# Kernel optimization log

Measured on AMD Instinct MI355X. Metric: run time of the kernel, lower is better.

Reference implementation:

```python
import jax, jax.numpy as jnp
import numpy as np

B, T, D, L = 64, 512, 1024, 32


def setup_inputs() -> dict:
    key = jax.random.key(0)
    ks = jax.random.split(key, 6)
    x = jax.random.normal(ks[0], (B, T, D), jnp.float32)
    W = jax.random.normal(ks[1], (D, L), jnp.float32) * 0.02  # TruncatedNormal(stddev=0.02) analogue
    b = jnp.zeros((L,), jnp.float32)
    transitions = jax.random.normal(ks[2], (L, L), jnp.float32) * 0.1
    label = jax.random.randint(ks[3], (B, T), 0, L).astype(jnp.int32)
    seqlen = jax.random.randint(ks[4], (B,), 1, T + 1).astype(jnp.int32)
    mask = jnp.arange(T)[None, :] < seqlen[:, None]
    return {"x": x, "W": W, "b": b, "transitions": transitions,
            "label": label, "seqlen": seqlen, "mask": mask}


def crf_sequence_score(emissions, label, seqlen, transitions):
    # emissions: [B,T,L]
    Bc, Tc, Lc = emissions.shape
    m = (jnp.arange(Tc)[None, :] < seqlen[:, None]).astype(emissions.dtype)  # [B,T]
    unary = jnp.take_along_axis(emissions, label[..., None].astype(jnp.int32), axis=-1)[..., 0]
    unary = jnp.sum(unary * m, axis=1)
    trans = transitions[label[:, :-1], label[:, 1:]]  # [B,T-1]
    mt = (jnp.arange(1, Tc)[None, :] < seqlen[:, None]).astype(emissions.dtype)
    binary = jnp.sum(trans * mt, axis=1)
    return unary + binary


def crf_log_norm(emissions, seqlen, transitions):
    Bc, Tc, Lc = emissions.shape
    alpha0 = emissions[:, 0]  # [B,L]
    valid = (jnp.arange(1, Tc)[None, :] < seqlen[:, None]).T  # [T-1,B]
    emits = jnp.moveaxis(emissions[:, 1:], 1, 0)  # [T-1,B,L]

    def step(alpha, inp):
        emit_t, v = inp
        new = jax.nn.logsumexp(alpha[:, :, None] + transitions[None], axis=1) + emit_t
        return jnp.where(v[:, None], new, alpha), None

    alpha, _ = jax.lax.scan(step, alpha0, (emits, valid))
    return jax.nn.logsumexp(alpha, axis=-1)  # [B]


def crf_decode(emissions, transitions, seqlen):
    Bc, Tc, Lc = emissions.shape
    alpha0 = emissions[:, 0]
    idx = jnp.arange(Lc, dtype=jnp.int32)
    valid = (jnp.arange(1, Tc)[None, :] < seqlen[:, None]).T  # [T-1,B]
    emits = jnp.moveaxis(emissions[:, 1:], 1, 0)

    def fwd(alpha, inp):
        emit_t, v = inp
        scores = alpha[:, :, None] + transitions[None]  # [B,L,L]
        best = jnp.max(scores, axis=1) + emit_t
        bp = jnp.argmax(scores, axis=1).astype(jnp.int32)  # [B,L]
        alpha_new = jnp.where(v[:, None], best, alpha)
        bp = jnp.where(v[:, None], bp, idx[None, :])  # identity bp on padded steps
        return alpha_new, bp

    alpha, bps = jax.lax.scan(fwd, alpha0, (emits, valid))  # bps: [T-1,B,L]
    last = jnp.argmax(alpha, axis=-1).astype(jnp.int32)  # [B]

    def bwd(tag, bp):
        prev = jnp.take_along_axis(bp, tag[:, None], axis=1)[:, 0]
        return prev, tag

    first, tags = jax.lax.scan(bwd, last, bps, reverse=True)  # tags[i] = tag at t=i+1
    seq = jnp.concatenate([first[None], tags], axis=0)  # [T,B]
    return jnp.moveaxis(seq, 0, 1)  # [B,T]


def reference(x, W, b, transitions, label, seqlen, mask):
    emissions = jnp.einsum('btd,dl->btl', x, W) + b  # Dense projection
    ll = crf_sequence_score(emissions, label, seqlen, transitions) - crf_log_norm(emissions, seqlen, transitions)
    loss = jnp.mean(-ll)
    vit = crf_decode(emissions, transitions, seqlen)
    tp = jnp.sum(((label > 0) & (vit == label)).astype(jnp.float32))
    tn = jnp.sum(((label > 0) & (vit != label)).astype(jnp.float32))
    fp = jnp.sum((mask & (label == 0) & (vit > 0)).astype(jnp.float32))
    return loss, vit, tp, tn, fp
```

## Files before the change

### kernel.cpp

```cpp
#include <hip/hip_runtime.h>
#include <stdint.h>
#include <math.h>

#define Bn 64
#define Tn 512
#define Dn 1024
#define Ln 32
#define LOG2E 1.4426950408889634f
#define LN2f  0.6931471805599453f

#define EMIS_OFF 0
#define LOGNORM_OFF (Bn * Tn * Ln)
#define SCORE_OFF (LOGNORM_OFF + Bn)
#define CNT_OFF (SCORE_OFF + Bn)

#define MAX3(a,b,c) fmaxf(fmaxf((a),(b)),(c))

template<int K>
__device__ __forceinline__ float rorf(float v) {
    return __int_as_float(__builtin_amdgcn_update_dpp(
        0, __float_as_int(v), 0x120 | K, 0xF, 0xF, true));
}

__device__ __forceinline__ float opaque_copy(float v) {
    float r;
    asm("v_mov_b32 %0, %1" : "=v"(r) : "v"(v));
    return r;
}

__device__ __forceinline__ void swap32p(float p, float& x, float& y) {
    x = p;
    y = opaque_copy(p);
    asm("v_permlane32_swap_b32 %0, %1" : "+v"(x), "+v"(y));
}
__device__ __forceinline__ void swap16p(float p, float& x, float& y) {
    x = p;
    y = opaque_copy(p);
    asm("v_permlane16_swap_b32 %0, %1" : "+v"(x), "+v"(y));
}

#define BM 128
#define KB 32
#define XSS 132

__global__ __launch_bounds__(256) void gemm_emis(
    const float* __restrict__ x, const float* __restrict__ Wm,
    const float* __restrict__ bias, const int* __restrict__ seqlen,
    float* __restrict__ emis)
{
    int b  = blockIdx.x >> 2;
    int t0 = (blockIdx.x & 3) * BM;
    if (t0 >= seqlen[b]) return;

    __shared__ __align__(16) float xs[KB * XSS];
    __shared__ __align__(16) float wsh[KB * Ln];

    int tid = threadIdx.x;
    int cg = tid & 7;
    int rg = tid >> 3;

    const float* xrow = x + (size_t)(b * Tn + t0) * Dn;

    float acc[4][4];
    #pragma unroll
    for (int z = 0; z < 4; z++)
        #pragma unroll
        for (int c = 0; c < 4; c++) acc[z][c] = 0.f;

    float4 xr[4]; float4 wr;
    #pragma unroll
    for (int u = 0; u < 4; u++) {
        int f = tid + 256 * u;
        xr[u] = *(const float4*)(xrow + (size_t)(f >> 3) * Dn + (f & 7) * 4);
    }
    wr = *(const float4*)(Wm + tid * 4);

    for (int k0 = 0; k0 < Dn; k0 += KB) {
        __syncthreads();
        #pragma unroll
        for (int u = 0; u < 4; u++) {
            int f = tid + 256 * u;
            int lrow = f >> 3, kk = f & 7;
            xs[(4 * kk + 0) * XSS + lrow] = xr[u].x;
            xs[(4 * kk + 1) * XSS + lrow] = xr[u].y;
            xs[(4 * kk + 2) * XSS + lrow] = xr[u].z;
            xs[(4 * kk + 3) * XSS + lrow] = xr[u].w;
        }
        *(float4*)(wsh + tid * 4) = wr;
        __syncthreads();

        int kn = k0 + KB;
        if (kn < Dn) {
            #pragma unroll
            for (int u = 0; u < 4; u++) {
                int f = tid + 256 * u;
                xr[u] = *(const float4*)(xrow + (size_t)(f >> 3) * Dn + kn + (f & 7) * 4);
            }
            wr = *(const float4*)(Wm + (size_t)kn * Ln + tid * 4);
        }

        #pragma unroll 8
        for (int k = 0; k < KB; k++) {
            float4 a = *(const float4*)(xs + k * XSS + 4 * rg);
            float4 w = *(const float4*)(wsh + k * Ln + 4 * cg);
            float av[4] = {a.x, a.y, a.z, a.w};
            float wv[4] = {w.x, w.y, w.z, w.w};
            #pragma unroll
            for (int z = 0; z < 4; z++)
                #pragma unroll
                for (int c = 0; c < 4; c++)
                    acc[z][c] = fmaf(av[z], wv[c], acc[z][c]);
        }
    }

    float4 bv = *(const float4*)(bias + 4 * cg);
    float bb[4] = {bv.x, bv.y, bv.z, bv.w};
    #pragma unroll
    for (int z = 0; z < 4; z++) {
        float4 o;
        o.x = acc[z][0] + bb[0];
        o.y = acc[z][1] + bb[1];
        o.z = acc[z][2] + bb[2];
        o.w = acc[z][3] + bb[3];
        *(float4*)(emis + (size_t)(b * Tn + t0 + 4 * rg + z) * Ln + 4 * cg) = o;
    }
}

#define CH 64

#define VIT_BODY(T, TRARR, SWAPFN, OE)                                       \
  {                                                                          \
    int tnx2 = ((T) + 2 < slen) ? ((T) + 2) : (slen - 1);                    \
    float e2n = es[tnx2 * Ln + (OE)];                                        \
    float vv0  = av            + TRARR[0];                                   \
    float vv1  = rorf<1>(av)   + TRARR[1];                                   \
    float vv2  = rorf<2>(av)   + TRARR[2];                                   \
    float vv3  = rorf<3>(av)   + TRARR[3];                                   \
    float vv4  = rorf<4>(av)   + TRARR[4];                                   \
    float vv5  = rorf<5>(av)   + TRARR[5];                                   \
    float vv6  = rorf<6>(av)   + TRARR[6];                                   \
    float vv7  = rorf<7>(av)   + TRARR[7];                                   \
    float vv8  = rorf<8>(av)   + TRARR[8];                                   \
    float vv9  = rorf<9>(av)   + TRARR[9];                                   \
    float vv10 = rorf<10>(av)  + TRARR[10];                                  \
    float vv11 = rorf<11>(av)  + TRARR[11];                                  \
    float vv12 = rorf<12>(av)  + TRARR[12];                                  \
    float vv13 = rorf<13>(av)  + TRARR[13];                                  \
    float vv14 = rorf<14>(av)  + TRARR[14];                                  \
    float vv15 = rorf<15>(av)  + TRARR[15];                                  \
    float g0 = MAX3(vv0,  vv1,  vv2);                                        \
    float g1 = MAX3(vv3,  vv4,  vv5);                                        \
    float g2 = MAX3(vv6,  vv7,  vv8);                                        \
    float g3 = MAX3(vv9,  vv10, vv11);                                       \
    float g4 = MAX3(vv12, vv13, vv14);                                       \
    float h0 = MAX3(g0, g1, g2);                                             \
    float h1 = MAX3(g3, g4, vv15);                                           \
    float p = fmaxf(h0, h1);                                                 \
    float xx, yy; SWAPFN(p, xx, yy);                                         \
    float cmb = fmaxf(xx, yy) + emit;                                        \
    al[(T) * Ln + (OE)] = cmb;                                               \
    av = cmb;                                                                \
    emit = emitn; emitn = e2n;                                               \
  }

#define LSE_BODY(T, EARR, SWAPFN, OE, DORENORM)                              \
  {                                                                          \
    int tnx2 = ((T) + 2 < slen) ? ((T) + 2) : (slen - 1);                    \
    float rawn = es[tnx2 * Ln + (OE)];                                       \
    float een = exp2f(rawnext * LOG2E);                                      \
    float s0 = a           * EARR[0];                                        \
    float s1 = rorf<1>(a)  * EARR[1];                                        \
    float s2 = rorf<2>(a)  * EARR[2];                                        \
    float s3 = rorf<3>(a)  * EARR[3];                                        \
    s0 = fmaf(rorf<4>(a),  EARR[4],  s0);                                    \
    s1 = fmaf(rorf<5>(a),  EARR[5],  s1);                                    \
    s2 = fmaf(rorf<6>(a),  EARR[6],  s2);                                    \
    s3 = fmaf(rorf<7>(a),  EARR[7],  s3);                                    \
    s0 = fmaf(rorf<8>(a),  EARR[8],  s0);                                    \
    s1 = fmaf(rorf<9>(a),  EARR[9],  s1);                                    \
    s2 = fmaf(rorf<10>(a), EARR[10], s2);                                    \
    s3 = fmaf(rorf<11>(a), EARR[11], s3);                                    \
    s0 = fmaf(rorf<12>(a), EARR[12], s0);                                    \
    s1 = fmaf(rorf<13>(a), EARR[13], s1);                                    \
    s2 = fmaf(rorf<14>(a), EARR[14], s2);                                    \
    s3 = fmaf(rorf<15>(a), EARR[15], s3);                                    \
    float pp = (s0 + s1) + (s2 + s3);                                        \
    float xx, yy; SWAPFN(pp, xx, yy);                                        \
    float s = (xx + yy) * eemit;                                             \
    if ((DORENORM) && (((T) & 3) == 0)) {                                    \
        unsigned sb = (unsigned)__builtin_amdgcn_readfirstlane(__float_as_int(s)); \
        int e = (int)((sb >> 23) & 0xFFu) - 127;                             \
        Eacc += e;                                                           \
        a = ldexpf(s, -e);                                                   \
    } else {                                                                 \
        a = s;                                                               \
    }                                                                        \
    eemit = een; rawnext = rawn;                                             \
  }

__global__ __launch_bounds__(512) void crf_forward(
    const float* __restrict__ emis, const float* __restrict__ trans,
    const int* __restrict__ label, const int* __restrict__ seqlen,
    float* __restrict__ out, float* __restrict__ wsf)
{
    __shared__ __align__(16) float es[Tn * Ln];
    __shared__ __align__(16) float al[Tn * Ln];
    __shared__ __align__(16) float trs[Ln * Ln];
    __shared__ uint8_t bp[Tn * Ln];
    __shared__ uint8_t Fm[16 * 32];
    __shared__ int btag[16];
    __shared__ int s_last;
    __shared__ float credA[8], credB[8], credC[8];

    int tid = threadIdx.x;
    int b = blockIdx.x;
    int slen = seqlen[b];
    int wv = tid >> 6;
    int lane = tid & 63;
    int j = lane & 31;

    const float* eb = emis + (size_t)b * Tn * Ln;

    {
        int n4 = slen * (Ln / 4);
        for (int i4 = tid; i4 < n4; i4 += 512)
            ((float4*)es)[i4] = ((const float4*)eb)[i4];
    }
    if (tid < 256) ((float4*)trs)[tid] = ((const float4*)trans)[tid];
    {
        uint32_t* bp32 = (uint32_t*)bp;
        for (int w = tid; w < Tn * Ln / 4; w += 512)
            bp32[w] = 0x03020100u + 0x04040404u * (uint32_t)(w & 7);
    }

    int rq[16];
    {
        float qf = (float)(lane & 15);
        rq[0]  = lane & 15;
        rq[1]  = (int)rorf<1>(qf);   rq[2]  = (int)rorf<2>(qf);
        rq[3]  = (int)rorf<3>(qf);   rq[4]  = (int)rorf<4>(qf);
        rq[5]  = (int)rorf<5>(qf);   rq[6]  = (int)rorf<6>(qf);
        rq[7]  = (int)rorf<7>(qf);   rq[8]  = (int)rorf<8>(qf);
        rq[9]  = (int)rorf<9>(qf);   rq[10] = (int)rorf<10>(qf);
        rq[11] = (int)rorf<11>(qf);  rq[12] = (int)rorf<12>(qf);
        rq[13] = (int)rorf<13>(qf);  rq[14] = (int)rorf<14>(qf);
        rq[15] = (int)rorf<15>(qf);
    }
    int q4  = lane & 15;
    int sb4 = (lane & 16) ? 16 : 0;
    int sb5 = (lane & 32) ? 16 : 0;
    int o4  = q4 + sb4;
    int o5  = q4 + sb5;

    __syncthreads();

    float av = 0.f, emit = 0.f, emitn = 0.f;
    float a = 0.f, eemit = 0.f, rawnext = 0.f;
    int   Eacc = 0;
    float trA[16], trB[16];
    float e2A[16], e2B[16];
    float trH[32];

    int i1 = (1 < slen) ? 1 : (slen - 1);
    int i2 = (2 < slen) ? 2 : (slen - 1);

    if (wv == 0) {
        #pragma unroll
        for (int k = 0; k < 16; k++) {
            trA[k] = trs[(rq[k] + sb5) * Ln + o4];
            trB[k] = trs[(rq[k] + sb4) * Ln + o5];
        }
        av = es[o5];
        al[o5] = av;
        emit  = es[i1 * Ln + o4];
        emitn = es[i2 * Ln + o5];
    } else if (wv == 1) {
        #pragma unroll
        for (int k = 0; k < 16; k++) {
            e2A[k] = exp2f(trs[(rq[k] + sb5) * Ln + o4] * LOG2E);
            e2B[k] = exp2f(trs[(rq[k] + sb4) * Ln + o5] * LOG2E);
        }
        a = exp2f(es[o5] * LOG2E);
        eemit   = exp2f(es[i1 * Ln + o4] * LOG2E);
        rawnext = es[i2 * Ln + o5];
    } else {
        #pragma unroll
        for (int i = 0; i < 32; i++) trH[i] = trs[i * Ln + j];
    }

    for (int c = 0; c < Tn / CH; c++) {
        int tb = (c == 0) ? 1 : c * CH;
        int te = (c + 1) * CH; if (te > slen) te = slen;

        if (wv == 0) {
            int t = tb;
            if ((t & 1) && t < te) { VIT_BODY(t, trA, swap32p, o4); t++; }
            for (; t + 1 < te; t += 2) {
                VIT_BODY(t,     trB, swap16p, o5);
                VIT_BODY(t + 1, trA, swap32p, o4);
            }
            if (t < te) { VIT_BODY(t, trB, swap16p, o5); }
        } else if (wv == 1) {
            int t = tb;
            if ((t & 1) && t < te) { LSE_BODY(t, e2A, swap32p, o4, 0); t++; }
            for (; t + 1 < te; t += 2) {
                LSE_BODY(t,     e2B, swap16p, o5, 1);
                LSE_BODY(t + 1, e2A, swap32p, o4, 0);
            }
            if (t < te) { LSE_BODY(t, e2B, swap16p, o5, 1); }
        } else if (c == 0) {
            if (wv == 2) {
                const int* lb = label + (size_t)b * Tn;
                float acc = 0.f;
                for (int t = lane; t < Tn; t += 64) {
                    if (t < slen) {
                        int lc = lb[t];
                        acc += es[t * Ln + lc];
                        if (t >= 1) acc += trs[lb[t - 1] * Ln + lc];
                    }
                }
                #pragma unroll
                for (int off = 32; off >= 1; off >>= 1) acc += __shfl_xor(acc, off);
                if (lane == 0) wsf[SCORE_OFF + b] = acc;
            }
        } else {
            int stripe = (wv - 2) * 2 + (lane >> 5);
            int pb = ((c - 1) == 0) ? 1 : (c - 1) * CH;
            int pe = c * CH; if (pe > slen) pe = slen;
            for (int t = pb + stripe; t < pe; t += 12) {
                const float* ar = al + (t - 1) * Ln;
                float vv[32];
                #pragma unroll
                for (int i = 0; i < 32; i += 4) {
                    float4 a4 = *(const float4*)(ar + i);
                    vv[i]     = a4.x + trH[i];
                    vv[i + 1] = a4.y + trH[i + 1];
                    vv[i + 2] = a4.z + trH[i + 2];
                    vv[i + 3] = a4.w + trH[i + 3];
                }
                float mv[16]; int mi[16];
                #pragma unroll
                for (int i = 0; i < 16; i++) {
                    bool g = vv[2*i+1] > vv[2*i];
                    mv[i] = g ? vv[2*i+1] : vv[2*i];
                    mi[i] = g ? (2*i+1) : (2*i);
                }
                #pragma unroll
                for (int i = 0; i < 8; i++) {
                    bool g = mv[2*i+1] > mv[2*i];
                    mv[i] = g ? mv[2*i+1] : mv[2*i];
                    mi[i] = g ? mi[2*i+1] : mi[2*i];
                }
                #pragma unroll
                for (int i = 0; i < 4; i++) {
                    bool g = mv[2*i+1] > mv[2*i];
                    mv[i] = g ? mv[2*i+1] : mv[2*i];
                    mi[i] = g ? mi[2*i+1] : mi[2*i];
                }
                #pragma unroll
                for (int i = 0; i < 2; i++) {
                    bool g = mv[2*i+1] > mv[2*i];
                    mv[i] = g ? mv[2*i+1] : mv[2*i];
                    mi[i] = g ? mi[2*i+1] : mi[2*i];
                }
                bp[t * Ln + j] = (uint8_t)mi[0];
            }
        }
        __syncthreads();
    }

    if (wv == 0) {
        int oT = ((slen - 1) & 1) ? o4 : o5;
        float mm = av; int ai = oT;
        #pragma unroll
        for (int off = 32; off >= 1; off >>= 1) {
            float om = __shfl_xor(mm, off);
            int   oi = __shfl_xor(ai, off);
            if (om > mm || (om == mm && oi < ai)) { mm = om; ai = oi; }
        }
        if (lane == 0) s_last = ai;
    } else if (wv == 1) {
        float ss = a;
        #pragma unroll
        for (int off = 32; off >= 1; off >>= 1) ss += __shfl_xor(ss, off);
        if (lane == 0)
            wsf[LOGNORM_OFF + b] = (log2f(ss) - 1.0f + (float)Eacc) * LN2f;
    } else {
        int stripe = (wv - 2) * 2 + (lane >> 5);
        int cc = Tn / CH - 1;
        int pb = cc * CH;
        int pe = Tn; if (pe > slen) pe = slen;
        for (int t = pb + stripe; t < pe; t += 12) {
            const float* ar = al + (t - 1) * Ln;
            float vv[32];
            #pragma unroll
            for (int i = 0; i < 32; i += 4) {
                float4 a4 = *(const float4*)(ar + i);
                vv[i]     = a4.x + trH[i];
                vv[i + 1] = a4.y + trH[i + 1];
                vv[i + 2] = a4.z + trH[i + 2];
                vv[i + 3] = a4.w + trH[i + 3];
            }
            float mv[16]; int mi[16];
            #pragma unroll
            for (int i = 0; i < 16; i++) {
                bool g = vv[2*i+1] > vv[2*i];
                mv[i] = g ? vv[2*i+1] : vv[2*i];
                mi[i] = g ? (2*i+1) : (2*i);
            }
            #pragma unroll
            for (int i = 0; i < 8; i++) {
                bool g = mv[2*i+1] > mv[2*i];
                mv[i] = g ? mv[2*i+1] : mv[2*i];
                mi[i] = g ? mi[2*i+1] : mi[2*i];
            }
            #pragma unroll
            for (int i = 0; i < 4; i++) {
                bool g = mv[2*i+1] > mv[2*i];
                mv[i] = g ? mv[2*i+1] : mv[2*i];
                mi[i] = g ? mi[2*i+1] : mi[2*i];
            }
            #pragma unroll
            for (int i = 0; i < 2; i++) {
                bool g = mv[2*i+1] > mv[2*i];
                mv[i] = g ? mv[2*i+1] : mv[2*i];
                mi[i] = g ? mi[2*i+1] : mi[2*i];
            }
            bp[t * Ln + j] = (uint8_t)mi[0];
        }
    }
    __syncthreads();

    int sseg = tid >> 5, ent = tid & 31;
    {
        int y = ent;
        for (int p = 32 * sseg + 31; p >= 32 * sseg; p--) y = bp[p * Ln + y];
        Fm[sseg * 32 + ent] = (uint8_t)y;
    }
    __syncthreads();
    if (tid == 0) {
        int y = s_last;
        btag[15] = y;
        for (int ss = 15; ss >= 1; ss--) { y = Fm[ss * 32 + y]; btag[ss - 1] = y; }
    }
    __syncthreads();
    int q = tid;
    int y = btag[sseg];
    for (int p = 32 * sseg + 31; p >= q + 1; p--) y = bp[p * Ln + y];
    out[1 + (size_t)b * Tn + q] = (float)y;

    int lbl = label[(size_t)b * Tn + q];
    float tpf = (lbl > 0 && y == lbl) ? 1.f : 0.f;
    float tnf = (lbl > 0 && y != lbl) ? 1.f : 0.f;
    float fpf = (q < slen && lbl == 0 && y > 0) ? 1.f : 0.f;
    #pragma unroll
    for (int off = 32; off >= 1; off >>= 1) {
        tpf += __shfl_xor(tpf, off);
        tnf += __shfl_xor(tnf, off);
        fpf += __shfl_xor(fpf, off);
    }
    if (lane == 0) { credA[wv] = tpf; credB[wv] = tnf; credC[wv] = fpf; }
    __syncthreads();
    if (tid == 0) {
        float aa = 0.f, bb2 = 0.f, cc2 = 0.f;
        #pragma unroll
        for (int w = 0; w < 8; w++) { aa += credA[w]; bb2 += credB[w]; cc2 += credC[w]; }
        wsf[CNT_OFF + b] = aa;
        wsf[CNT_OFF + Bn + b] = bb2;
        wsf[CNT_OFF + 2 * Bn + b] = cc2;
    }
}

__global__ __launch_bounds__(64) void crf_final(const float* __restrict__ wsf,
                                                float* __restrict__ out)
{
    int lane = threadIdx.x;
    float nll = wsf[LOGNORM_OFF + lane] - wsf[SCORE_OFF + lane];
    float tp = wsf[CNT_OFF + lane];
    float tn = wsf[CNT_OFF + Bn + lane];
    float fp = wsf[CNT_OFF + 2 * Bn + lane];
    #pragma unroll
    for (int off = 32; off >= 1; off >>= 1) {
        nll += __shfl_xor(nll, off);
        tp  += __shfl_xor(tp, off);
        tn  += __shfl_xor(tn, off);
        fp  += __shfl_xor(fp, off);
    }
    if (lane == 0) {
        out[0] = nll * (1.f / 64.f);
        out[1 + Bn * Tn + 0] = tp;
        out[1 + Bn * Tn + 1] = tn;
        out[1 + Bn * Tn + 2] = fp;
    }
}

extern "C" void kernel_launch(void* const* d_in, const int* in_sizes, int n_in,
                              void* d_out, int out_size, void* d_ws, size_t ws_size,
                              hipStream_t stream) {
    const float* x     = (const float*)d_in[0];
    const float* W     = (const float*)d_in[1];
    const float* bias  = (const float*)d_in[2];
    const float* trans = (const float*)d_in[3];
    const int* label   = (const int*)d_in[4];
    const int* seqlen  = (const int*)d_in[5];
    float* out = (float*)d_out;
    float* wsf = (float*)d_ws;

    gemm_emis<<<dim3(Bn * (Tn / BM)), dim3(256), 0, stream>>>(x, W, bias, seqlen, wsf + EMIS_OFF);
    crf_forward<<<dim3(Bn), dim3(512), 0, stream>>>(wsf + EMIS_OFF, trans, label, seqlen, out, wsf);
    crf_final<<<dim3(1), dim3(64), 0, stream>>>(wsf, out);
}
```

Measured before the change: 271.7 us.

## Halve GEMM row tile and restrict backpointer work to four helper waves

The emission GEMM now uses 64-row tiles instead of 128. That doubles the grid to 512 blocks for better CU coverage and finer skipping of padded timesteps, at the cost of less register reuse per thread. In the CRF forward kernel, backpointer recomputation moves from six helper waves to four (waves 2,3,6,7) with stride 8, and waves 4 and 5 sit idle. This may reduce contention with the latency-critical recurrence waves, but it gives each helper lane more timesteps to process.

```diff
diff --git a/kernel.cpp b/kernel.cpp
--- a/kernel.cpp
+++ b/kernel.cpp
@@ -39,20 +39,20 @@
     asm("v_permlane16_swap_b32 %0, %1" : "+v"(x), "+v"(y));
 }
 
-#define BM 128
+#define BM2 64
 #define KB 32
-#define XSS 132
+#define XS2 68
 
 __global__ __launch_bounds__(256) void gemm_emis(
     const float* __restrict__ x, const float* __restrict__ Wm,
     const float* __restrict__ bias, const int* __restrict__ seqlen,
     float* __restrict__ emis)
 {
-    int b  = blockIdx.x >> 2;
-    int t0 = (blockIdx.x & 3) * BM;
+    int b  = blockIdx.x >> 3;
+    int t0 = (blockIdx.x & 7) * BM2;
     if (t0 >= seqlen[b]) return;
 
-    __shared__ __align__(16) float xs[KB * XSS];
+    __shared__ __align__(16) float xs[KB * XS2];
     __shared__ __align__(16) float wsh[KB * Ln];
 
     int tid = threadIdx.x;
@@ -61,15 +61,15 @@
 
     const float* xrow = x + (size_t)(b * Tn + t0) * Dn;
 
-    float acc[4][4];
+    float acc[2][4];
     #pragma unroll
-    for (int z = 0; z < 4; z++)
+    for (int z = 0; z < 2; z++)
         #pragma unroll
         for (int c = 0; c < 4; c++) acc[z][c] = 0.f;
 
-    float4 xr[4]; float4 wr;
+    float4 xr[2]; float4 wr;
     #pragma unroll
-    for (int u = 0; u < 4; u++) {
+    for (int u = 0; u < 2; u++) {
         int f = tid + 256 * u;
         xr[u] = *(const float4*)(xrow + (size_t)(f >> 3) * Dn + (f & 7) * 4);
     }
@@ -78,13 +78,13 @@
     for (int k0 = 0; k0 < Dn; k0 += KB) {
         __syncthreads();
         #pragma unroll
-        for (int u = 0; u < 4; u++) {
+        for (int u = 0; u < 2; u++) {
             int f = tid + 256 * u;
             int lrow = f >> 3, kk = f & 7;
-            xs[(4 * kk + 0) * XSS + lrow] = xr[u].x;
-            xs[(4 * kk + 1) * XSS + lrow] = xr[u].y;
-            xs[(4 * kk + 2) * XSS + lrow] = xr[u].z;
-            xs[(4 * kk + 3) * XSS + lrow] = xr[u].w;
+            xs[(4 * kk + 0) * XS2 + lrow] = xr[u].x;
+            xs[(4 * kk + 1) * XS2 + lrow] = xr[u].y;
+            xs[(4 * kk + 2) * XS2 + lrow] = xr[u].z;
+            xs[(4 * kk + 3) * XS2 + lrow] = xr[u].w;
         }
         *(float4*)(wsh + tid * 4) = wr;
         __syncthreads();
@@ -92,7 +92,7 @@
         int kn = k0 + KB;
         if (kn < Dn) {
             #pragma unroll
-            for (int u = 0; u < 4; u++) {
+            for (int u = 0; u < 2; u++) {
                 int f = tid + 256 * u;
                 xr[u] = *(const float4*)(xrow + (size_t)(f >> 3) * Dn + kn + (f & 7) * 4);
             }
@@ -101,12 +101,12 @@
 
         #pragma unroll 8
         for (int k = 0; k < KB; k++) {
-            float4 a = *(const float4*)(xs + k * XSS + 4 * rg);
+            float2 a2 = *(const float2*)(xs + k * XS2 + 2 * rg);
             float4 w = *(const float4*)(wsh + k * Ln + 4 * cg);
-            float av[4] = {a.x, a.y, a.z, a.w};
+            float av[2] = {a2.x, a2.y};
             float wv[4] = {w.x, w.y, w.z, w.w};
             #pragma unroll
-            for (int z = 0; z < 4; z++)
+            for (int z = 0; z < 2; z++)
                 #pragma unroll
                 for (int c = 0; c < 4; c++)
                     acc[z][c] = fmaf(av[z], wv[c], acc[z][c]);
@@ -116,13 +116,13 @@
     float4 bv = *(const float4*)(bias + 4 * cg);
     float bb[4] = {bv.x, bv.y, bv.z, bv.w};
     #pragma unroll
-    for (int z = 0; z < 4; z++) {
+    for (int z = 0; z < 2; z++) {
         float4 o;
         o.x = acc[z][0] + bb[0];
         o.y = acc[z][1] + bb[1];
         o.z = acc[z][2] + bb[2];
         o.w = acc[z][3] + bb[3];
-        *(float4*)(emis + (size_t)(b * Tn + t0 + 4 * rg + z) * Ln + 4 * cg) = o;
+        *(float4*)(emis + (size_t)(b * Tn + t0 + 2 * rg + z) * Ln + 4 * cg) = o;
     }
 }
 
@@ -198,6 +198,46 @@
     eemit = een; rawnext = rawn;                                             \
   }
 
+#define BP_LOOP(PB, PE, STRIDE)                                              \
+    for (int t = (PB); t < (PE); t += (STRIDE)) {                            \
+        const float* ar = al + (t - 1) * Ln;                                 \
+        float vv[32];                                                        \
+        _Pragma("unroll")                                                    \
+        for (int i = 0; i < 32; i += 4) {                                    \
+            float4 a4 = *(const float4*)(ar + i);                            \
+            vv[i]     = a4.x + trH[i];                                       \
+            vv[i + 1] = a4.y + trH[i + 1];                                   \
+            vv[i + 2] = a4.z + trH[i + 2];                                   \
+            vv[i + 3] = a4.w + trH[i + 3];                                   \
+        }                                                                    \
+        float mv[16]; int mi[16];                                            \
+        _Pragma("unroll")                                                    \
+        for (int i = 0; i < 16; i++) {                                       \
+            bool g = vv[2*i+1] > vv[2*i];                                    \
+            mv[i] = g ? vv[2*i+1] : vv[2*i];                                 \
+            mi[i] = g ? (2*i+1) : (2*i);                                     \
+        }                                                                    \
+        _Pragma("unroll")                                                    \
+        for (int i = 0; i < 8; i++) {                                        \
+            bool g = mv[2*i+1] > mv[2*i];                                    \
+            mv[i] = g ? mv[2*i+1] : mv[2*i];                                 \
+            mi[i] = g ? mi[2*i+1] : mi[2*i];                                 \
+        }                                                                    \
+        _Pragma("unroll")                                                    \
+        for (int i = 0; i < 4; i++) {                                        \
+            bool g = mv[2*i+1] > mv[2*i];                                    \
+            mv[i] = g ? mv[2*i+1] : mv[2*i];                                 \
+            mi[i] = g ? mi[2*i+1] : mi[2*i];                                 \
+        }                                                                    \
+        _Pragma("unroll")                                                    \
+        for (int i = 0; i < 2; i++) {                                        \
+            bool g = mv[2*i+1] > mv[2*i];                                    \
+            mv[i] = g ? mv[2*i+1] : mv[2*i];                                 \
+            mi[i] = g ? mi[2*i+1] : mi[2*i];                                 \
+        }                                                                    \
+        bp[t * Ln + j] = (uint8_t)mi[0];                                     \
+    }
+
 __global__ __launch_bounds__(512) void crf_forward(
     const float* __restrict__ emis, const float* __restrict__ trans,
     const int* __restrict__ label, const int* __restrict__ seqlen,
@@ -264,6 +304,10 @@
     int i1 = (1 < slen) ? 1 : (slen - 1);
     int i2 = (2 < slen) ? 2 : (slen - 1);
 
+    bool isHelper = (wv == 2) || (wv == 3) || (wv == 6) || (wv == 7);
+    int hw = (wv >= 6) ? (wv - 4) : (wv - 2);
+    int stripe = hw * 2 + (lane >> 5);
+
     if (wv == 0) {
         #pragma unroll
         for (int k = 0; k < 16; k++) {
@@ -283,7 +327,7 @@
         a = exp2f(es[o5] * LOG2E);
         eemit   = exp2f(es[i1 * Ln + o4] * LOG2E);
         rawnext = es[i2 * Ln + o5];
-    } else {
+    } else if (isHelper) {
         #pragma unroll
         for (int i = 0; i < 32; i++) trH[i] = trs[i * Ln + j];
     }
@@ -308,6 +352,7 @@
                 LSE_BODY(t + 1, e2A, swap32p, o4, 0);
             }
             if (t < te) { LSE_BODY(t, e2B, swap16p, o5, 1); }
+        } else if (!isHelper) {
         } else if (c == 0) {
             if (wv == 2) {
                 const int* lb = label + (size_t)b * Tn;
@@ -324,47 +369,9 @@
                 if (lane == 0) wsf[SCORE_OFF + b] = acc;
             }
         } else {
-            int stripe = (wv - 2) * 2 + (lane >> 5);
             int pb = ((c - 1) == 0) ? 1 : (c - 1) * CH;
             int pe = c * CH; if (pe > slen) pe = slen;
-            for (int t = pb + stripe; t < pe; t += 12) {
-                const float* ar = al + (t - 1) * Ln;
-                float vv[32];
-                #pragma unroll
-                for (int i = 0; i < 32; i += 4) {
-                    float4 a4 = *(const float4*)(ar + i);
-                    vv[i]     = a4.x + trH[i];
-                    vv[i + 1] = a4.y + trH[i + 1];
-                    vv[i + 2] = a4.z + trH[i + 2];
-                    vv[i + 3] = a4.w + trH[i + 3];
-                }
-                float mv[16]; int mi[16];
-                #pragma unroll
-                for (int i = 0; i < 16; i++) {
-                    bool g = vv[2*i+1] > vv[2*i];
-                    mv[i] = g ? vv[2*i+1] : vv[2*i];
-                    mi[i] = g ? (2*i+1) : (2*i);
-                }
-                #pragma unroll
-                for (int i = 0; i < 8; i++) {
-                    bool g = mv[2*i+1] > mv[2*i];
-                    mv[i] = g ? mv[2*i+1] : mv[2*i];
-                    mi[i] = g ? mi[2*i+1] : mi[2*i];
-                }
-                #pragma unroll
-                for (int i = 0; i < 4; i++) {
-                    bool g = mv[2*i+1] > mv[2*i];
-                    mv[i] = g ? mv[2*i+1] : mv[2*i];
-                    mi[i] = g ? mi[2*i+1] : mi[2*i];
-                }
-                #pragma unroll
-                for (int i = 0; i < 2; i++) {
-                    bool g = mv[2*i+1] > mv[2*i];
-                    mv[i] = g ? mv[2*i+1] : mv[2*i];
-                    mi[i] = g ? mi[2*i+1] : mi[2*i];
-                }
-                bp[t * Ln + j] = (uint8_t)mi[0];
-            }
+            BP_LOOP(pb + stripe, pe, 8)
         }
         __syncthreads();
     }
@@ -385,49 +392,11 @@
         for (int off = 32; off >= 1; off >>= 1) ss += __shfl_xor(ss, off);
         if (lane == 0)
             wsf[LOGNORM_OFF + b] = (log2f(ss) - 1.0f + (float)Eacc) * LN2f;
-    } else {
-        int stripe = (wv - 2) * 2 + (lane >> 5);
+    } else if (isHelper) {
         int cc = Tn / CH - 1;
         int pb = cc * CH;
         int pe = Tn; if (pe > slen) pe = slen;
-        for (int t = pb + stripe; t < pe; t += 12) {
-            const float* ar = al + (t - 1) * Ln;
-            float vv[32];
-            #pragma unroll
-            for (int i = 0; i < 32; i += 4) {
-                float4 a4 = *(const float4*)(ar + i);
-                vv[i]     = a4.x + trH[i];
-                vv[i + 1] = a4.y + trH[i + 1];
-                vv[i + 2] = a4.z + trH[i + 2];
-                vv[i + 3] = a4.w + trH[i + 3];
-            }
-            float mv[16]; int mi[16];
-            #pragma unroll
-            for (int i = 0; i < 16; i++) {
-                bool g = vv[2*i+1] > vv[2*i];
-                mv[i] = g ? vv[2*i+1] : vv[2*i];
-                mi[i] = g ? (2*i+1) : (2*i);
-            }
-            #pragma unroll
-            for (int i = 0; i < 8; i++) {
-                bool g = mv[2*i+1] > mv[2*i];
-                mv[i] = g ? mv[2*i+1] : mv[2*i];
-                mi[i] = g ? mi[2*i+1] : mi[2*i];
-            }
-            #pragma unroll
-            for (int i = 0; i < 4; i++) {
-                bool g = mv[2*i+1] > mv[2*i];
-                mv[i] = g ? mv[2*i+1] : mv[2*i];
-                mi[i] = g ? mi[2*i+1] : mi[2*i];
-            }
-            #pragma unroll
-            for (int i = 0; i < 2; i++) {
-                bool g = mv[2*i+1] > mv[2*i];
-                mv[i] = g ? mv[2*i+1] : mv[2*i];
-                mi[i] = g ? mi[2*i+1] : mi[2*i];
-            }
-            bp[t * Ln + j] = (uint8_t)mi[0];
-        }
+        BP_LOOP(pb + stripe, pe, 8)
     }
     __syncthreads();
 
@@ -506,7 +475,7 @@
     float* out = (float*)d_out;
     float* wsf = (float*)d_ws;
 
-    gemm_emis<<<dim3(Bn * (Tn / BM)), dim3(256), 0, stream>>>(x, W, bias, seqlen, wsf + EMIS_OFF);
+    gemm_emis<<<dim3(Bn * (Tn / BM2)), dim3(256), 0, stream>>>(x, W, bias, seqlen, wsf + EMIS_OFF);
     crf_forward<<<dim3(Bn), dim3(512), 0, stream>>>(wsf + EMIS_OFF, trans, label, seqlen, out, wsf);
     crf_final<<<dim3(1), dim3(64), 0, stream>>>(wsf, out);
 }
```

Result: slower. 284.5 us (+4.7%).
